# Kernel optimization log

Hardware: AMD Instinct MI355X
Metric: run time of the kernel (lower is better)

## Reference

```python
import jax, jax.numpy as jnp
import numpy as np

N_NODES = 100000
N_EDGES = 1600000
D = 128
N_LAYERS = 3  # GIN num_layers = n_layers + 1 with n_layers = 2
BN_EPS = 1e-5


def _batchnorm(x, gamma, beta):
    # Training-mode BatchNorm1d over the node axis (biased variance, as torch uses
    # for normalization).
    mean = jnp.mean(x, axis=0)
    var = jnp.mean((x - mean) ** 2, axis=0)
    return (x - mean) * jax.lax.rsqrt(var + BN_EPS) * gamma + beta


def setup_inputs() -> dict:
    key = jax.random.key(0)
    ks = jax.random.split(key, 5)
    features = jax.random.normal(ks[0], (N_NODES, D), dtype=jnp.float32)
    W = jax.random.normal(ks[1], (N_LAYERS, D, D), dtype=jnp.float32) * 0.05
    b = jnp.zeros((N_LAYERS, D), dtype=jnp.float32)
    eps = jnp.zeros((N_LAYERS,), dtype=jnp.float32)  # learn_eps init 0
    bn1_gamma = jnp.ones((N_LAYERS, D), dtype=jnp.float32)
    bn1_beta = jnp.zeros((N_LAYERS, D), dtype=jnp.float32)
    bn2_gamma = jnp.ones((N_LAYERS, D), dtype=jnp.float32)
    bn2_beta = jnp.zeros((N_LAYERS, D), dtype=jnp.float32)
    src = jax.random.randint(ks[2], (N_EDGES,), 0, N_NODES, dtype=jnp.int64 if jax.config.jax_enable_x64 else jnp.int32)
    dst = jax.random.randint(ks[3], (N_EDGES,), 0, N_NODES, dtype=jnp.int64 if jax.config.jax_enable_x64 else jnp.int32)
    return {
        'features': features, 'W': W, 'b': b, 'eps': eps,
        'bn1_gamma': bn1_gamma, 'bn1_beta': bn1_beta,
        'bn2_gamma': bn2_gamma, 'bn2_beta': bn2_beta,
        'src': src, 'dst': dst,
    }


def reference(features, W, b, eps, bn1_gamma, bn1_beta, bn2_gamma, bn2_beta, src, dst):
    n = features.shape[0]
    h = features
    hidden_rep = [h]
    for i in range(N_LAYERS):
        # GINConv, 'sum' aggregation: (1+eps)*h_v + sum_{u->v} h_u
        agg = jax.ops.segment_sum(h[src], dst, num_segments=n)
        z = (1.0 + eps[i]) * h + agg
        # ApplyNodeFunc: Linear (num_mlp_layers=1) -> BN -> ReLU
        z = z @ W[i] + b[i]
        z = jax.nn.relu(_batchnorm(z, bn1_gamma[i], bn1_beta[i]))
        # GIN.forward: outer BN -> ReLU
        z = jax.nn.relu(_batchnorm(z, bn2_gamma[i], bn2_beta[i]))
        h = z
        hidden_rep.append(h)
    # torch.stack(hidden_rep) -> [n_layers+2, N, D]
    return jnp.stack(hidden_rep, axis=0)
```

## Files before the change

### kernel.cpp

```cpp
#include <hip/hip_runtime.h>
#include <hip/hip_bf16.h>

#define DD 128

typedef __attribute__((ext_vector_type(8))) short bfrag8;
typedef __attribute__((ext_vector_type(4))) float f32x4;

__device__ __forceinline__ float bf16lo(unsigned int u) {
    union { unsigned int i; float f; } c; c.i = u << 16; return c.f;
}
__device__ __forceinline__ float bf16hi(unsigned int u) {
    union { unsigned int i; float f; } c; c.i = u & 0xffff0000u; return c.f;
}
__device__ __forceinline__ float bf16f(unsigned short u) {
    union { unsigned int i; float f; } c; c.i = ((unsigned int)u) << 16; return c.f;
}
__device__ __forceinline__ unsigned short f2bf(float f) {
    union { float f; unsigned int i; } c; c.f = f;
    unsigned int x = c.i;
    unsigned int r = (x + 0x7fffu + ((x >> 16) & 1u)) >> 16;
    return (unsigned short)r;
}

__global__ void k_setup(const int* __restrict__ dst, int* __restrict__ deg, int E,
                        const float* __restrict__ features, float* __restrict__ out0,
                        unsigned int* __restrict__ hb, int total4,
                        const float* __restrict__ W, unsigned short* __restrict__ Wt) {
    int gtid = blockIdx.x * blockDim.x + threadIdx.x;
    int gsz = gridDim.x * blockDim.x;
    for (int i = gtid; i < E; i += gsz) atomicAdd(&deg[dst[i]], 1);
    for (int i = gtid; i < total4; i += gsz) {
        float4 v = ((const float4*)features)[i];
        ((float4*)out0)[i] = v;
        unsigned int lo = (unsigned int)f2bf(v.x) | ((unsigned int)f2bf(v.y) << 16);
        unsigned int hi = (unsigned int)f2bf(v.z) | ((unsigned int)f2bf(v.w) << 16);
        ((uint2*)hb)[i] = make_uint2(lo, hi);
    }
    for (int i = gtid; i < 3 * 128 * 128; i += gsz) {
        int l = i >> 14, r = i & 16383, k = r >> 7, n = r & 127;
        Wt[(l << 14) + n * 128 + k] = f2bf(W[i]);
    }
}

__global__ void k_scan1(const int* __restrict__ deg, int* __restrict__ partials, int Nn) {
    __shared__ int sm[256];
    int tid = threadIdx.x;
    int base = (blockIdx.x << 10) + 4 * tid;
    int s = 0;
    if (base + 3 < Nn) {
        int4 v = *(const int4*)&deg[base];
        s = v.x + v.y + v.z + v.w;
    } else {
        for (int j = 0; j < 4; j++) if (base + j < Nn) s += deg[base + j];
    }
    sm[tid] = s;
    __syncthreads();
    for (int off = 128; off > 0; off >>= 1) {
        if (tid < off) sm[tid] += sm[tid + off];
        __syncthreads();
    }
    if (tid == 0) partials[blockIdx.x] = sm[0];
}

__global__ void k_scan3(const int* __restrict__ deg, const int* __restrict__ partials,
                        int* __restrict__ row_start, int Nn, int E, int nchunk) {
    __shared__ int sp[256];
    __shared__ int sm[256];
    int tid = threadIdx.x, c = blockIdx.x;
    int p = (tid < nchunk) ? partials[tid] : 0;
    sp[tid] = p;
    __syncthreads();
    for (int off = 1; off < 256; off <<= 1) {
        int t = (tid >= off) ? sp[tid - off] : 0;
        __syncthreads();
        sp[tid] += t;
        __syncthreads();
    }
    int chunkpref = (c == 0) ? 0 : sp[c - 1];

    int base = (c << 10) + 4 * tid;
    int d0 = 0, d1 = 0, d2 = 0, d3 = 0;
    if (base + 3 < Nn) {
        int4 v = *(const int4*)&deg[base];
        d0 = v.x; d1 = v.y; d2 = v.z; d3 = v.w;
    } else {
        if (base + 0 < Nn) d0 = deg[base + 0];
        if (base + 1 < Nn) d1 = deg[base + 1];
        if (base + 2 < Nn) d2 = deg[base + 2];
        if (base + 3 < Nn) d3 = deg[base + 3];
    }
    int ts = d0 + d1 + d2 + d3;
    sm[tid] = ts;
    __syncthreads();
    for (int off = 1; off < 256; off <<= 1) {
        int t = (tid >= off) ? sm[tid - off] : 0;
        __syncthreads();
        sm[tid] += t;
        __syncthreads();
    }
    int run = chunkpref + sm[tid] - ts;
    if (base + 0 < Nn) row_start[base + 0] = run; run += d0;
    if (base + 1 < Nn) row_start[base + 1] = run; run += d1;
    if (base + 2 < Nn) row_start[base + 2] = run; run += d2;
    if (base + 3 < Nn) row_start[base + 3] = run;
    if (c == 0 && tid == 0) row_start[Nn] = E;
}

__global__ void k_scatter(const int* __restrict__ src, const int* __restrict__ dst,
                          const int* __restrict__ row_start, int* __restrict__ cursor,
                          int* __restrict__ csr, int E) {
    int i = blockIdx.x * blockDim.x + threadIdx.x;
    if (i < E) {
        int d = dst[i];
        int pos = row_start[d] + atomicAdd(&cursor[d], 1);
        csr[pos] = src[i];
    }
}

__launch_bounds__(256)
__global__ void k_gg(const unsigned int* __restrict__ hb, const int* __restrict__ row_start,
                     const int* __restrict__ csr, const float* __restrict__ eps, int layer,
                     const unsigned short* __restrict__ Wt, const float* __restrict__ bias,
                     unsigned short* __restrict__ yb, float* __restrict__ stl, int Nn) {
    __shared__ unsigned short Al[64 * 136];
    int tid = threadIdx.x;
    int m0 = blockIdx.x * 64;
    int wv = tid >> 6, lane = tid & 63;

    float e1 = 1.0f + eps[layer];
    for (int r8 = 0; r8 < 16; r8++) {
        int r = (wv << 4) + r8;
        int v = m0 + r;
        unsigned int packed = 0;
        if (v < Nn) {
            unsigned int hs = hb[(size_t)v * 64 + lane];
            float ax = e1 * bf16lo(hs);
            float ay = e1 * bf16hi(hs);
            int beg = row_start[v], end = row_start[v + 1];
            int e = beg;
            for (; e + 7 < end; e += 8) {
                int u0 = csr[e], u1 = csr[e + 1], u2 = csr[e + 2], u3 = csr[e + 3];
                int u4 = csr[e + 4], u5 = csr[e + 5], u6 = csr[e + 6], u7 = csr[e + 7];
                unsigned int h0 = hb[(size_t)u0 * 64 + lane];
                unsigned int h1 = hb[(size_t)u1 * 64 + lane];
                unsigned int h2 = hb[(size_t)u2 * 64 + lane];
                unsigned int h3 = hb[(size_t)u3 * 64 + lane];
                unsigned int h4 = hb[(size_t)u4 * 64 + lane];
                unsigned int h5 = hb[(size_t)u5 * 64 + lane];
                unsigned int h6 = hb[(size_t)u6 * 64 + lane];
                unsigned int h7 = hb[(size_t)u7 * 64 + lane];
                ax += bf16lo(h0) + bf16lo(h1) + bf16lo(h2) + bf16lo(h3)
                    + bf16lo(h4) + bf16lo(h5) + bf16lo(h6) + bf16lo(h7);
                ay += bf16hi(h0) + bf16hi(h1) + bf16hi(h2) + bf16hi(h3)
                    + bf16hi(h4) + bf16hi(h5) + bf16hi(h6) + bf16hi(h7);
            }
            for (; e < end; e++) {
                unsigned int hu = hb[(size_t)csr[e] * 64 + lane];
                ax += bf16lo(hu); ay += bf16hi(hu);
            }
            packed = (unsigned int)f2bf(ax) | ((unsigned int)f2bf(ay) << 16);
        }
        *(unsigned int*)&Al[r * 136 + 2 * lane] = packed;
    }
    __syncthreads();

    int tcol = lane & 15, quad = lane >> 4;
    const unsigned short* Wl = Wt + (layer << 14);
    f32x4 acc[4][2];
    #pragma unroll
    for (int a = 0; a < 4; a++)
        #pragma unroll
        for (int b2 = 0; b2 < 2; b2++) acc[a][b2] = (f32x4){0.f, 0.f, 0.f, 0.f};

    #pragma unroll
    for (int kk = 0; kk < 128; kk += 32) {
        int kb = kk + quad * 8;
        bfrag8 af[4], bf[2];
        #pragma unroll
        for (int mt = 0; mt < 4; mt++)
            af[mt] = *(const bfrag8*)&Al[(16 * mt + tcol) * 136 + kb];
        #pragma unroll
        for (int nt = 0; nt < 2; nt++)
            bf[nt] = *(const bfrag8*)&Wl[(32 * wv + 16 * nt + tcol) * 128 + kb];
        #pragma unroll
        for (int mt = 0; mt < 4; mt++)
            #pragma unroll
            for (int nt = 0; nt < 2; nt++)
                acc[mt][nt] = __builtin_amdgcn_mfma_f32_16x16x32_bf16(af[mt], bf[nt], acc[mt][nt], 0, 0, 0);
    }

    #pragma unroll
    for (int nt = 0; nt < 2; nt++) {
        int col = 32 * wv + 16 * nt + tcol;
        float bcol = bias[layer * 128 + col];
        float psum = 0.f, psq = 0.f;
        #pragma unroll
        for (int mt = 0; mt < 4; mt++) {
            #pragma unroll
            for (int r = 0; r < 4; r++) {
                int row = m0 + 16 * mt + quad * 4 + r;
                if (row < Nn) {
                    unsigned short u = f2bf(acc[mt][nt][r] + bcol);
                    yb[(size_t)row * 128 + col] = u;
                    float vr = bf16f(u);
                    psum += vr;
                    psq += vr * vr;
                }
            }
        }
        psum += __shfl_xor(psum, 16); psq += __shfl_xor(psq, 16);
        psum += __shfl_xor(psum, 32); psq += __shfl_xor(psq, 32);
        if (lane < 16) {
            atomicAdd(&stl[col], psum);
            atomicAdd(&stl[128 + col], psq);
        }
    }
}

__launch_bounds__(256)
__global__ void k_stats2(const unsigned short* __restrict__ yb, float* __restrict__ stl,
                         const float* __restrict__ g1, const float* __restrict__ b1,
                         int layer, int totalU8, float invN) {
    __shared__ float red[512];
    int tid = threadIdx.x;
    if (tid < 128) {
        float m = stl[tid] * invN;
        float var = stl[128 + tid] * invN - m * m;
        float rstd = rsqrtf(var + 1e-5f);
        float s = g1[layer * 128 + tid] * rstd;
        red[tid] = s;
        red[128 + tid] = b1[layer * 128 + tid] - m * s;
        red[256 + tid] = 0.f;
        red[384 + tid] = 0.f;
    }
    __syncthreads();
    int lane = tid & 63;
    int cbase = (8 * tid) & 127;
    float s1r[8], sh1r[8];
    #pragma unroll
    for (int j = 0; j < 8; j++) { s1r[j] = red[cbase + j]; sh1r[j] = red[128 + cbase + j]; }
    float ps[8], pq[8];
    #pragma unroll
    for (int j = 0; j < 8; j++) { ps[j] = 0.f; pq[j] = 0.f; }
    int gtid = blockIdx.x * 256 + tid;
    int gsz = gridDim.x * 256;
    const uint4* yb4 = (const uint4*)yb;
    for (int i = gtid; i < totalU8; i += gsz) {
        uint4 v = yb4[i];
        float f[8];
        f[0] = bf16lo(v.x); f[1] = bf16hi(v.x);
        f[2] = bf16lo(v.y); f[3] = bf16hi(v.y);
        f[4] = bf16lo(v.z); f[5] = bf16hi(v.z);
        f[6] = bf16lo(v.w); f[7] = bf16hi(v.w);
        #pragma unroll
        for (int j = 0; j < 8; j++) {
            float t = fmaxf(f[j] * s1r[j] + sh1r[j], 0.f);
            ps[j] += t; pq[j] += t * t;
        }
    }
    #pragma unroll
    for (int j = 0; j < 8; j++) {
        ps[j] += __shfl_xor(ps[j], 16);
        pq[j] += __shfl_xor(pq[j], 16);
        ps[j] += __shfl_xor(ps[j], 32);
        pq[j] += __shfl_xor(pq[j], 32);
    }
    if (lane < 16) {
        #pragma unroll
        for (int j = 0; j < 8; j++) {
            atomicAdd(&red[256 + cbase + j], ps[j]);
            atomicAdd(&red[384 + cbase + j], pq[j]);
        }
    }
    __syncthreads();
    if (tid < 128) {
        atomicAdd(&stl[256 + tid], red[256 + tid]);
        atomicAdd(&stl[384 + tid], red[384 + tid]);
    }
}

__launch_bounds__(256)
__global__ void k_apply(const unsigned short* __restrict__ yb, const float* __restrict__ stl,
                        const float* __restrict__ g1, const float* __restrict__ b1,
                        const float* __restrict__ g2, const float* __restrict__ b2,
                        int layer, float* __restrict__ outl, unsigned int* __restrict__ hb,
                        int totalU8, float invN) {
    __shared__ float red[512];
    int tid = threadIdx.x;
    if (tid < 128) {
        float m1 = stl[tid] * invN;
        float v1 = stl[128 + tid] * invN - m1 * m1;
        float r1 = rsqrtf(v1 + 1e-5f);
        float s1 = g1[layer * 128 + tid] * r1;
        red[tid] = s1;
        red[128 + tid] = b1[layer * 128 + tid] - m1 * s1;
        float m2 = stl[256 + tid] * invN;
        float v2 = stl[384 + tid] * invN - m2 * m2;
        float r2 = rsqrtf(v2 + 1e-5f);
        float s2 = g2[layer * 128 + tid] * r2;
        red[256 + tid] = s2;
        red[384 + tid] = b2[layer * 128 + tid] - m2 * s2;
    }
    __syncthreads();
    int cbase = (8 * tid) & 127;
    float s1a[8], sh1a[8], s2a[8], sh2a[8];
    #pragma unroll
    for (int j = 0; j < 8; j++) {
        s1a[j]  = red[cbase + j];       sh1a[j] = red[128 + cbase + j];
        s2a[j]  = red[256 + cbase + j]; sh2a[j] = red[384 + cbase + j];
    }
    int gtid = blockIdx.x * 256 + tid;
    int gsz = gridDim.x * 256;
    const uint4* yb4 = (const uint4*)yb;
    for (int i = gtid; i < totalU8; i += gsz) {
        uint4 v = yb4[i];
        float f[8];
        f[0] = bf16lo(v.x); f[1] = bf16hi(v.x);
        f[2] = bf16lo(v.y); f[3] = bf16hi(v.y);
        f[4] = bf16lo(v.z); f[5] = bf16hi(v.z);
        f[6] = bf16lo(v.w); f[7] = bf16hi(v.w);
        float o[8];
        #pragma unroll
        for (int j = 0; j < 8; j++) {
            float t = fmaxf(f[j] * s1a[j] + sh1a[j], 0.f);
            o[j] = fmaxf(t * s2a[j] + sh2a[j], 0.f);
        }
        ((float4*)outl)[2 * i]     = make_float4(o[0], o[1], o[2], o[3]);
        ((float4*)outl)[2 * i + 1] = make_float4(o[4], o[5], o[6], o[7]);
        uint4 hbv;
        hbv.x = (unsigned int)f2bf(o[0]) | ((unsigned int)f2bf(o[1]) << 16);
        hbv.y = (unsigned int)f2bf(o[2]) | ((unsigned int)f2bf(o[3]) << 16);
        hbv.z = (unsigned int)f2bf(o[4]) | ((unsigned int)f2bf(o[5]) << 16);
        hbv.w = (unsigned int)f2bf(o[6]) | ((unsigned int)f2bf(o[7]) << 16);
        ((uint4*)hb)[i] = hbv;
    }
}

extern "C" void kernel_launch(void* const* d_in, const int* in_sizes, int n_in,
                              void* d_out, int out_size, void* d_ws, size_t ws_size,
                              hipStream_t stream) {
    const float* features = (const float*)d_in[0];
    const float* W        = (const float*)d_in[1];
    const float* bias     = (const float*)d_in[2];
    const float* eps      = (const float*)d_in[3];
    const float* g1       = (const float*)d_in[4];
    const float* b1       = (const float*)d_in[5];
    const float* g2       = (const float*)d_in[6];
    const float* b2       = (const float*)d_in[7];
    const int*   src      = (const int*)d_in[8];
    const int*   dst      = (const int*)d_in[9];

    const int Nn = in_sizes[0] / DD;
    const int E  = in_sizes[8];
    float* out = (float*)d_out;

    char* w = (char*)d_ws;
    auto alloc = [&](size_t bytes) -> char* {
        char* p = w;
        w += (bytes + 255) & ~(size_t)255;
        return p;
    };
    int*   deg    = (int*)alloc((size_t)Nn * 4);
    int*   cursor = (int*)alloc((size_t)Nn * 4);
    float* stats  = (float*)alloc(3 * 512 * 4);
    char*  zero_end = w;
    int* row_start = (int*)alloc((size_t)(Nn + 1) * 4);
    int* partials  = (int*)alloc(1024);
    int* csr       = (int*)alloc((size_t)E * 4);
    unsigned int* hb = (unsigned int*)alloc((size_t)Nn * 64 * 4);
    unsigned short* Wt = (unsigned short*)alloc((size_t)3 * 128 * 128 * 2);
    unsigned short* yb = (unsigned short*)alloc((size_t)Nn * 128 * 2);

    const int total4 = Nn * DD / 4;
    const int totalU8 = Nn * DD / 8;
    const float invN = 1.0f / (float)Nn;
    const int nchunk = (Nn + 1023) / 1024;

    hipMemsetAsync(deg, 0, (size_t)(zero_end - (char*)deg), stream);

    k_setup<<<(E + 255) / 256, 256, 0, stream>>>(dst, deg, E, features, out, hb, total4, W, Wt);
    k_scan1<<<nchunk, 256, 0, stream>>>(deg, partials, Nn);
    k_scan3<<<nchunk, 256, 0, stream>>>(deg, partials, row_start, Nn, E, nchunk);
    k_scatter<<<(E + 255) / 256, 256, 0, stream>>>(src, dst, row_start, cursor, csr, E);

    for (int l = 0; l < 3; l++) {
        float* stl = stats + l * 512;
        float* outl = out + (size_t)(l + 1) * Nn * DD;
        k_gg<<<(Nn + 63) / 64, 256, 0, stream>>>(hb, row_start, csr, eps, l, Wt, bias, yb, stl, Nn);
        k_stats2<<<512, 256, 0, stream>>>(yb, stl, g1, b1, l, totalU8, invN);
        k_apply<<<1024, 256, 0, stream>>>(yb, stl, g1, b1, g2, b2, l, outl, hb, totalU8, invN);
    }
}
```

Before: 955.4 us.

## Split fused gather+GEMM kernel into separate gather and GEMM kernels

Unfuses the neighbor aggregation from the MFMA GEMM kernel: a new gather kernel assigns one wavefront per node across many small blocks and writes the aggregated bf16 rows to a new buffer, and the GEMM kernel loads them with vectorized loads into shared memory. This is meant to spread the latency-bound gather over far more blocks and waves instead of 16 serial rows per wave, with the GEMM no longer stalled on gathers. In exchange it adds an extra global write and read of the aggregated matrix and one more launch per layer.

```diff
diff --git a/kernel.cpp b/kernel.cpp
--- a/kernel.cpp
+++ b/kernel.cpp
@@ -117,53 +117,60 @@
     }
 }
 
+__global__ void k_gather(const unsigned int* __restrict__ hb, const int* __restrict__ row_start,
+                         const int* __restrict__ csr, const float* __restrict__ eps, int layer,
+                         unsigned int* __restrict__ zb, int Nn) {
+    int wv = threadIdx.x >> 6, lane = threadIdx.x & 63;
+    int v = blockIdx.x * 4 + wv;
+    if (v >= Nn) return;
+    float e1 = 1.0f + eps[layer];
+    unsigned int hs = hb[(size_t)v * 64 + lane];
+    float ax = e1 * bf16lo(hs);
+    float ay = e1 * bf16hi(hs);
+    int beg = row_start[v], end = row_start[v + 1];
+    int e = beg;
+    for (; e + 7 < end; e += 8) {
+        int u0 = csr[e], u1 = csr[e + 1], u2 = csr[e + 2], u3 = csr[e + 3];
+        int u4 = csr[e + 4], u5 = csr[e + 5], u6 = csr[e + 6], u7 = csr[e + 7];
+        unsigned int h0 = hb[(size_t)u0 * 64 + lane];
+        unsigned int h1 = hb[(size_t)u1 * 64 + lane];
+        unsigned int h2 = hb[(size_t)u2 * 64 + lane];
+        unsigned int h3 = hb[(size_t)u3 * 64 + lane];
+        unsigned int h4 = hb[(size_t)u4 * 64 + lane];
+        unsigned int h5 = hb[(size_t)u5 * 64 + lane];
+        unsigned int h6 = hb[(size_t)u6 * 64 + lane];
+        unsigned int h7 = hb[(size_t)u7 * 64 + lane];
+        ax += bf16lo(h0) + bf16lo(h1) + bf16lo(h2) + bf16lo(h3)
+            + bf16lo(h4) + bf16lo(h5) + bf16lo(h6) + bf16lo(h7);
+        ay += bf16hi(h0) + bf16hi(h1) + bf16hi(h2) + bf16hi(h3)
+            + bf16hi(h4) + bf16hi(h5) + bf16hi(h6) + bf16hi(h7);
+    }
+    for (; e < end; e++) {
+        unsigned int hu = hb[(size_t)csr[e] * 64 + lane];
+        ax += bf16lo(hu); ay += bf16hi(hu);
+    }
+    zb[(size_t)v * 64 + lane] = (unsigned int)f2bf(ax) | ((unsigned int)f2bf(ay) << 16);
+}
+
 __launch_bounds__(256)
-__global__ void k_gg(const unsigned int* __restrict__ hb, const int* __restrict__ row_start,
-                     const int* __restrict__ csr, const float* __restrict__ eps, int layer,
-                     const unsigned short* __restrict__ Wt, const float* __restrict__ bias,
-                     unsigned short* __restrict__ yb, float* __restrict__ stl, int Nn) {
+__global__ void k_gemm(const unsigned short* __restrict__ zb, const unsigned short* __restrict__ Wt,
+                       const float* __restrict__ bias, int layer, unsigned short* __restrict__ yb,
+                       float* __restrict__ stl, int Nn) {
     __shared__ unsigned short Al[64 * 136];
     int tid = threadIdx.x;
     int m0 = blockIdx.x * 64;
-    int wv = tid >> 6, lane = tid & 63;
-
-    float e1 = 1.0f + eps[layer];
-    for (int r8 = 0; r8 < 16; r8++) {
-        int r = (wv << 4) + r8;
-        int v = m0 + r;
-        unsigned int packed = 0;
-        if (v < Nn) {
-            unsigned int hs = hb[(size_t)v * 64 + lane];
-            float ax = e1 * bf16lo(hs);
-            float ay = e1 * bf16hi(hs);
-            int beg = row_start[v], end = row_start[v + 1];
-            int e = beg;
-            for (; e + 7 < end; e += 8) {
-                int u0 = csr[e], u1 = csr[e + 1], u2 = csr[e + 2], u3 = csr[e + 3];
-                int u4 = csr[e + 4], u5 = csr[e + 5], u6 = csr[e + 6], u7 = csr[e + 7];
-                unsigned int h0 = hb[(size_t)u0 * 64 + lane];
-                unsigned int h1 = hb[(size_t)u1 * 64 + lane];
-                unsigned int h2 = hb[(size_t)u2 * 64 + lane];
-                unsigned int h3 = hb[(size_t)u3 * 64 + lane];
-                unsigned int h4 = hb[(size_t)u4 * 64 + lane];
-                unsigned int h5 = hb[(size_t)u5 * 64 + lane];
-                unsigned int h6 = hb[(size_t)u6 * 64 + lane];
-                unsigned int h7 = hb[(size_t)u7 * 64 + lane];
-                ax += bf16lo(h0) + bf16lo(h1) + bf16lo(h2) + bf16lo(h3)
-                    + bf16lo(h4) + bf16lo(h5) + bf16lo(h6) + bf16lo(h7);
-                ay += bf16hi(h0) + bf16hi(h1) + bf16hi(h2) + bf16hi(h3)
-                    + bf16hi(h4) + bf16hi(h5) + bf16hi(h6) + bf16hi(h7);
-            }
-            for (; e < end; e++) {
-                unsigned int hu = hb[(size_t)csr[e] * 64 + lane];
-                ax += bf16lo(hu); ay += bf16hi(hu);
-            }
-            packed = (unsigned int)f2bf(ax) | ((unsigned int)f2bf(ay) << 16);
-        }
-        *(unsigned int*)&Al[r * 136 + 2 * lane] = packed;
-    }
-    __syncthreads();
-
+    #pragma unroll
+    for (int p = 0; p < 4; p++) {
+        int slot = p * 256 + tid;
+        int r = slot >> 4, c = slot & 15;
+        int grow = m0 + r;
+        uint4 val = make_uint4(0, 0, 0, 0);
+        if (grow < Nn) val = *(const uint4*)&zb[(size_t)grow * 128 + c * 8];
+        *(uint4*)&Al[r * 136 + c * 8] = val;
+    }
+    __syncthreads();
+
+    int lane = tid & 63, wv = tid >> 6;
     int tcol = lane & 15, quad = lane >> 4;
     const unsigned short* Wl = Wt + (layer << 14);
     f32x4 acc[4][2];
@@ -368,6 +375,7 @@
     int* partials  = (int*)alloc(1024);
     int* csr       = (int*)alloc((size_t)E * 4);
     unsigned int* hb = (unsigned int*)alloc((size_t)Nn * 64 * 4);
+    unsigned int* zb = (unsigned int*)alloc((size_t)Nn * 64 * 4);
     unsigned short* Wt = (unsigned short*)alloc((size_t)3 * 128 * 128 * 2);
     unsigned short* yb = (unsigned short*)alloc((size_t)Nn * 128 * 2);
 
@@ -386,7 +394,9 @@
     for (int l = 0; l < 3; l++) {
         float* stl = stats + l * 512;
         float* outl = out + (size_t)(l + 1) * Nn * DD;
-        k_gg<<<(Nn + 63) / 64, 256, 0, stream>>>(hb, row_start, csr, eps, l, Wt, bias, yb, stl, Nn);
+        k_gather<<<(Nn + 3) / 4, 256, 0, stream>>>(hb, row_start, csr, eps, l, zb, Nn);
+        k_gemm<<<(Nn + 63) / 64, 256, 0, stream>>>((const unsigned short*)zb, Wt, bias, l, yb,
+                                                   stl, Nn);
         k_stats2<<<512, 256, 0, stream>>>(yb, stl, g1, b1, l, totalU8, invN);
         k_apply<<<1024, 256, 0, stream>>>(yb, stl, g1, b1, g2, b2, l, outl, hb, totalU8, invN);
     }
```

New measurement: 863.8 us. 9.6% less time.
